# Kernel optimization log

Hardware: AMD Instinct MI355X
Metric: run time of the kernel (lower is better)

The kernel has to match this reference:

```python
import jax, jax.numpy as jnp
import numpy as np

B, C, L = 8, 128, 16384
K, STRIDE, PAD = 7, 3, 3
IC = 64  # intermediate_channels
CK = C * K  # 896 patch channels


def setup_inputs() -> dict:
    key = jax.random.key(0)
    ks = jax.random.split(key, 5)
    x = jax.random.normal(ks[0], (B, C, L), dtype=jnp.float32)
    W1 = jax.random.normal(ks[1], (IC, CK), dtype=jnp.float32) * (1.0 / np.sqrt(CK))
    b1 = jax.random.normal(ks[2], (IC,), dtype=jnp.float32) * 0.01
    W2 = jax.random.normal(ks[3], (CK, IC), dtype=jnp.float32) * (1.0 / np.sqrt(IC))
    b2 = jax.random.normal(ks[4], (CK,), dtype=jnp.float32) * 0.01
    return {"x": x, "W1": W1, "b1": b1, "W2": W2, "b2": b2}


def reference(x, W1, b1, W2, b2):
    b, c, l = x.shape
    lp = l + 2 * PAD
    # 1) circular pad along length
    xp = jnp.concatenate([x[..., -PAD:], x, x[..., :PAD]], axis=-1)  # (B,C,Lp)
    # 2) unfold: sliding windows of size K, stride STRIDE
    P = (lp - K) // STRIDE + 1
    idx = jnp.arange(P)[:, None] * STRIDE + jnp.arange(K)[None, :]  # (P,K)
    win = xp[:, :, idx]  # (B,C,P,K)
    # torch Unfold channel ordering: (B, C*K, P) with K fastest within channel
    patches = jnp.transpose(win, (0, 1, 3, 2)).reshape(b, c * K, P)
    # 3) 1x1-conv MLP on patch features
    h = jax.nn.relu(jnp.einsum('oc,bcp->bop', W1, patches) + b1[None, :, None])
    y = jnp.einsum('oc,bcp->bop', W2, h) + b2[None, :, None]  # (B, C*K, P)
    # 4) fold: overlap-add back to (B,C,Lp)
    vals = jnp.transpose(y.reshape(b, c, K, P), (0, 1, 3, 2))  # (B,C,P,K)
    folded = jnp.zeros((b, c, lp), dtype=x.dtype).at[:, :, idx].add(vals)
    # 5) ReplicationPad2d((0,0,1,1)) on height-1 tensor + mean over height=3:
    #    three identical rows averaged -> identity, preserved without materializing.
    # 6) crop back to original length
    return folded[:, :, PAD:PAD + l]
```

## Files before the change

### kernel.cpp

```cpp
#include <hip/hip_runtime.h>
#include <hip/hip_bf16.h>

#define B_    8
#define C_    128
#define L_    16384
#define K_    7
#define IC_   64
#define CK_   896
#define P_    5462
#define NP_   32
#define NT1_  171
#define NPOS_ 100
#define LDW_  136
#define HROWS 5480
#define HBSTR (HROWS * 64)

using bf16x8 = __attribute__((ext_vector_type(8))) __bf16;
using bf16x4 = __attribute__((ext_vector_type(4))) __bf16;
using f32x4  = __attribute__((ext_vector_type(4))) float;

#define W1KB_OFF  0
#define W2RB_OFF  114688
#define B2SUM_OFF 262144
#define B2TAB_OFF 263680
#define HTAB_OFF  270336

__global__ void prep_kernel(const float* __restrict__ W1, const float* __restrict__ W2,
                            const float* __restrict__ b2, __bf16* __restrict__ W1kb,
                            __bf16* __restrict__ W2rb, float* __restrict__ B2sum,
                            float* __restrict__ B2tab) {
    int idx = blockIdx.x * blockDim.x + threadIdx.x;
    int stride = gridDim.x * blockDim.x;
    for (int i = idx; i < 7 * 64 * 128; i += stride) {
        int k = i >> 13, o = (i >> 7) & 63, c = i & 127;
        W1kb[i] = (__bf16)W1[o * CK_ + c * 7 + k];
    }
    for (int i = idx; i < 3 * 128 * 3 * 64; i += stride) {
        int o = i & 63, t = (i >> 6) % 3, c = (i / 192) & 127, r = i / 24576;
        int kk = r + 3 * t;
        W2rb[i] = (kk <= 6) ? (__bf16)W2[(c * 7 + kk) * 64 + o] : (__bf16)0.0f;
    }
    for (int i = idx; i < 3 * 3 * 128; i += stride) {
        int c = i & 127, t = (i >> 7) % 3, r = i / 384;
        int kk = r + 3 * t;
        B2tab[i] = (kk <= 6) ? b2[c * 7 + kk] : 0.0f;
    }
    for (int i = idx; i < 3 * 128; i += stride) {
        int c = i & 127, r = i >> 7;
        float s = 0.0f;
        for (int t = 0; t < 3; ++t) { int kk = r + 3 * t; if (kk <= 6) s += b2[c * 7 + kk]; }
        B2sum[i] = s;
    }
}

__global__ __launch_bounds__(256, 4)
void conv1_kernel(const float* __restrict__ x, const float* __restrict__ b1,
                  const __bf16* __restrict__ W1kb, __bf16* __restrict__ hTab) {
    __shared__ __align__(16) __bf16 winT[NPOS_][LDW_];

    const int tid  = threadIdx.x;
    const int lane = tid & 63;
    const int w    = tid >> 6;
    const int row  = lane & 15;
    const int g    = lane >> 4;
    const int tile = blockIdx.x;
    const int b    = blockIdx.y;
    const int p0   = tile * NP_;
    const int gx0  = 3 * p0 - 3;

    __bf16* hb = hTab + (size_t)b * HBSTR;
    if (tile == 0 && tid < 64) reinterpret_cast<int*>(hb)[tid] = 0;

    const size_t xbase = ((size_t)b * C_) << 14;
    #pragma unroll
    for (int oc = 0; oc < 4; ++oc) {
        int c0 = (w * 4 + oc) * 8;
        const float* xr = x + xbase + ((size_t)c0 << 14);
        #pragma unroll
        for (int it = 0; it < 2; ++it) {
            int i = lane + (it << 6);
            if (i < NPOS_) {
                int xi = gx0 + i;
                xi += (xi < 0) ? L_ : 0;
                xi -= (xi >= L_) ? L_ : 0;
                bf16x8 pk;
                #pragma unroll
                for (int j = 0; j < 8; ++j)
                    pk[j] = (__bf16)xr[((size_t)j << 14) + xi];
                *reinterpret_cast<bf16x8*>(&winT[i][c0]) = pk;
            }
        }
    }

    __syncthreads();

    const bf16x8* W1v = reinterpret_cast<const bf16x8*>(W1kb);
    f32x4 acc1[2];
    #pragma unroll
    for (int pt = 0; pt < 2; ++pt) acc1[pt] = (f32x4){0.f, 0.f, 0.f, 0.f};
    #pragma unroll
    for (int k = 0; k < 7; ++k) {
        #pragma unroll
        for (int cs = 0; cs < 4; ++cs) {
            bf16x8 a = W1v[(k * 64 + w * 16 + row) * 16 + cs * 4 + g];
            #pragma unroll
            for (int pt = 0; pt < 2; ++pt) {
                const bf16x8 bfr = *reinterpret_cast<const bf16x8*>(
                    &winT[3 * (pt * 16 + row) + k][cs * 32 + g * 8]);
                acc1[pt] = __builtin_amdgcn_mfma_f32_16x16x32_bf16(a, bfr, acc1[pt], 0, 0, 0);
            }
        }
    }

    f32x4 b1v = *reinterpret_cast<const f32x4*>(b1 + w * 16 + g * 4);
    #pragma unroll
    for (int pt = 0; pt < 2; ++pt) {
        int pl = pt * 16 + row;
        int p  = p0 + pl;
        bool pvalid = (p < P_);
        bf16x4 hq;
        #pragma unroll
        for (int i = 0; i < 4; ++i) {
            float v = acc1[pt][i] + b1v[i];
            v = fmaxf(v, 0.0f);
            hq[i] = pvalid ? (__bf16)v : (__bf16)0.0f;
        }
        *reinterpret_cast<bf16x4*>(hb + (size_t)(p + 2) * 64 + w * 16 + g * 4) = hq;
    }
}

__global__ __launch_bounds__(256, 4)
void conv2_kernel(const __bf16* __restrict__ hTab, const __bf16* __restrict__ W2rb,
                  const float* __restrict__ B2sum, const float* __restrict__ B2tab,
                  float* __restrict__ out) {
    const int tid  = threadIdx.x;
    const int lane = tid & 63;
    const int w    = tid >> 6;
    const int row  = lane & 15;
    const int g    = lane >> 4;
    const int gx   = blockIdx.x;
    const int ch   = blockIdx.y;
    const int b    = blockIdx.z;

    const int ct = ch * 4 + w;
    const int c0 = ct * 16 + g * 4;

    const bf16x8* W2v = reinterpret_cast<const bf16x8*>(W2rb);
    bf16x8 af2[14];
    {
        int idx = 0;
        #pragma unroll
        for (int r = 0; r < 3; ++r) {
            const int ntt = (r == 0) ? 3 : 2;
            #pragma unroll
            for (int t = 0; t < 3; ++t) {
                if (t < ntt) {
                    #pragma unroll
                    for (int os = 0; os < 2; ++os) {
                        af2[idx] = W2v[((r * 128 + ct * 16 + row) * 3 + t) * 8 + os * 4 + g];
                        idx++;
                    }
                }
            }
        }
    }
    f32x4 bs[3];
    #pragma unroll
    for (int r = 0; r < 3; ++r)
        bs[r] = *reinterpret_cast<const f32x4*>(B2sum + r * 128 + c0);

    const __bf16* hb = hTab + (size_t)b * HBSTR;
    const size_t obase = ((size_t)b * C_) << 14;

    #pragma unroll
    for (int j = 0; j < 4; ++j) {
        const int qt = gx * 4 + j;
        const int q0 = qt * 16;
        if (q0 > P_) continue;

        bf16x8 bq[3][2];
        #pragma unroll
        for (int t = 0; t < 3; ++t)
            #pragma unroll
            for (int os = 0; os < 2; ++os)
                bq[t][os] = *reinterpret_cast<const bf16x8*>(
                    hb + (size_t)(q0 + row + 2 - t) * 64 + os * 32 + g * 8);

        const int q = q0 + row;
        f32x4 acc3[3];
        {
            int idx = 0;
            #pragma unroll
            for (int r = 0; r < 3; ++r) {
                acc3[r] = (f32x4){0.f, 0.f, 0.f, 0.f};
                const int ntt = (r == 0) ? 3 : 2;
                #pragma unroll
                for (int t = 0; t < 3; ++t) {
                    if (t < ntt) {
                        #pragma unroll
                        for (int os = 0; os < 2; ++os) {
                            acc3[r] = __builtin_amdgcn_mfma_f32_16x16x32_bf16(
                                af2[idx], bq[t][os], acc3[r], 0, 0, 0);
                            idx++;
                        }
                    }
                }
            }
        }

        const bool edge = (qt == 0) || (qt == 341);
        if (!edge) {
            #pragma unroll
            for (int i = 0; i < 4; ++i) {
                const int c = c0 + i;
                float* p = out + obase + (((size_t)c) << 14) + (3 * q - 3);
                p[0] = acc3[0][i] + bs[0][i];
                p[1] = acc3[1][i] + bs[1][i];
                p[2] = acc3[2][i] + bs[2][i];
            }
        } else {
            if (q >= 1 && q <= P_) {
                #pragma unroll
                for (int i = 0; i < 4; ++i) {
                    const int c = c0 + i;
                    float bv[3] = {0.f, 0.f, 0.f};
                    #pragma unroll
                    for (int r = 0; r < 3; ++r) {
                        const int ntt = (r == 0) ? 3 : 2;
                        #pragma unroll
                        for (int t = 0; t < 3; ++t) {
                            if (t < ntt && (unsigned)(q - t) < (unsigned)P_)
                                bv[r] += B2tab[(r * 3 + t) * 128 + c];
                        }
                    }
                    float* p = out + obase + (((size_t)c) << 14) + (3 * q - 3);
                    if (q <= P_ - 1) {
                        p[0] = acc3[0][i] + bv[0];
                        p[1] = acc3[1][i] + bv[1];
                        p[2] = acc3[2][i] + bv[2];
                    } else {
                        p[0] = acc3[0][i] + bv[0];
                    }
                }
            }
        }
    }
}

extern "C" void kernel_launch(void* const* d_in, const int* in_sizes, int n_in,
                              void* d_out, int out_size, void* d_ws, size_t ws_size,
                              hipStream_t stream) {
    const float* x  = (const float*)d_in[0];
    const float* W1 = (const float*)d_in[1];
    const float* b1 = (const float*)d_in[2];
    const float* W2 = (const float*)d_in[3];
    const float* b2 = (const float*)d_in[4];
    float* out = (float*)d_out;
    char* ws = (char*)d_ws;
    __bf16* W1kb = (__bf16*)(ws + W1KB_OFF);
    __bf16* W2rb = (__bf16*)(ws + W2RB_OFF);
    float* B2sum = (float*)(ws + B2SUM_OFF);
    float* B2tab = (float*)(ws + B2TAB_OFF);
    __bf16* hTab = (__bf16*)(ws + HTAB_OFF);

    prep_kernel<<<64, 256, 0, stream>>>(W1, W2, b2, W1kb, W2rb, B2sum, B2tab);
    conv1_kernel<<<dim3(NT1_, B_), 256, 0, stream>>>(x, b1, W1kb, hTab);
    conv2_kernel<<<dim3(86, 2, B_), 256, 0, stream>>>(hTab, W2rb, B2sum, B2tab, out);
}
```

Measured before the change: 82.42 us.

## Halve conv1 tile size and load x with vectorized float4 channel-pair reads

Conv1 now covers 16 patches per block instead of 32, doubling the grid and raising the occupancy hint to 8 blocks per SM. The x staging loop changes from scalar per-position strided loads to float4 loads along length for pairs of channels, writing bf16 pairs into the transposed shared window. The goal is better global load coalescing and more parallelism. The cost is more halo overlap between tiles and fewer MFMAs per block to amortise the W1 fragment loads.

```diff
diff --git a/kernel.cpp b/kernel.cpp
--- a/kernel.cpp
+++ b/kernel.cpp
@@ -8,15 +8,16 @@
 #define IC_   64
 #define CK_   896
 #define P_    5462
-#define NP_   32
-#define NT1_  171
-#define NPOS_ 100
+#define NP_   16
+#define NT1_  342
+#define NPOS_ 52
 #define LDW_  136
 #define HROWS 5480
 #define HBSTR (HROWS * 64)
 
 using bf16x8 = __attribute__((ext_vector_type(8))) __bf16;
 using bf16x4 = __attribute__((ext_vector_type(4))) __bf16;
+using bf16x2 = __attribute__((ext_vector_type(2))) __bf16;
 using f32x4  = __attribute__((ext_vector_type(4))) float;
 
 #define W1KB_OFF  0
@@ -53,7 +54,7 @@
     }
 }
 
-__global__ __launch_bounds__(256, 4)
+__global__ __launch_bounds__(256, 8)
 void conv1_kernel(const float* __restrict__ x, const float* __restrict__ b1,
                   const __bf16* __restrict__ W1kb, __bf16* __restrict__ hTab) {
     __shared__ __align__(16) __bf16 winT[NPOS_][LDW_];
@@ -67,27 +68,32 @@
     const int b    = blockIdx.y;
     const int p0   = tile * NP_;
     const int gx0  = 3 * p0 - 3;
+    const int ax0  = gx0 - 1;
 
     __bf16* hb = hTab + (size_t)b * HBSTR;
     if (tile == 0 && tid < 64) reinterpret_cast<int*>(hb)[tid] = 0;
 
     const size_t xbase = ((size_t)b * C_) << 14;
-    #pragma unroll
-    for (int oc = 0; oc < 4; ++oc) {
-        int c0 = (w * 4 + oc) * 8;
-        const float* xr = x + xbase + ((size_t)c0 << 14);
-        #pragma unroll
-        for (int it = 0; it < 2; ++it) {
-            int i = lane + (it << 6);
-            if (i < NPOS_) {
-                int xi = gx0 + i;
+    {
+        const int c2 = lane * 2;
+        const float* xr0 = x + xbase + ((size_t)c2 << 14);
+        #pragma unroll
+        for (int jq = 0; jq < 4; ++jq) {
+            int q = w * 4 + jq;
+            if (q < 14) {
+                int xi = ax0 + q * 4;
                 xi += (xi < 0) ? L_ : 0;
                 xi -= (xi >= L_) ? L_ : 0;
-                bf16x8 pk;
+                f32x4 va = *reinterpret_cast<const f32x4*>(xr0 + xi);
+                f32x4 vb = *reinterpret_cast<const f32x4*>(xr0 + L_ + xi);
                 #pragma unroll
-                for (int j = 0; j < 8; ++j)
-                    pk[j] = (__bf16)xr[((size_t)j << 14) + xi];
-                *reinterpret_cast<bf16x8*>(&winT[i][c0]) = pk;
+                for (int j = 0; j < 4; ++j) {
+                    int pos = q * 4 + j - 1;
+                    if ((unsigned)pos < (unsigned)NPOS_) {
+                        bf16x2 pk; pk[0] = (__bf16)va[j]; pk[1] = (__bf16)vb[j];
+                        *reinterpret_cast<bf16x2*>(&winT[pos][c2]) = pk;
+                    }
+                }
             }
         }
     }
@@ -95,33 +101,26 @@
     __syncthreads();
 
     const bf16x8* W1v = reinterpret_cast<const bf16x8*>(W1kb);
-    f32x4 acc1[2];
-    #pragma unroll
-    for (int pt = 0; pt < 2; ++pt) acc1[pt] = (f32x4){0.f, 0.f, 0.f, 0.f};
+    f32x4 acc1 = (f32x4){0.f, 0.f, 0.f, 0.f};
     #pragma unroll
     for (int k = 0; k < 7; ++k) {
         #pragma unroll
         for (int cs = 0; cs < 4; ++cs) {
             bf16x8 a = W1v[(k * 64 + w * 16 + row) * 16 + cs * 4 + g];
-            #pragma unroll
-            for (int pt = 0; pt < 2; ++pt) {
-                const bf16x8 bfr = *reinterpret_cast<const bf16x8*>(
-                    &winT[3 * (pt * 16 + row) + k][cs * 32 + g * 8]);
-                acc1[pt] = __builtin_amdgcn_mfma_f32_16x16x32_bf16(a, bfr, acc1[pt], 0, 0, 0);
-            }
+            const bf16x8 bfr = *reinterpret_cast<const bf16x8*>(
+                &winT[3 * row + k][cs * 32 + g * 8]);
+            acc1 = __builtin_amdgcn_mfma_f32_16x16x32_bf16(a, bfr, acc1, 0, 0, 0);
         }
     }
 
     f32x4 b1v = *reinterpret_cast<const f32x4*>(b1 + w * 16 + g * 4);
-    #pragma unroll
-    for (int pt = 0; pt < 2; ++pt) {
-        int pl = pt * 16 + row;
-        int p  = p0 + pl;
+    {
+        int p = p0 + row;
         bool pvalid = (p < P_);
         bf16x4 hq;
         #pragma unroll
         for (int i = 0; i < 4; ++i) {
-            float v = acc1[pt][i] + b1v[i];
+            float v = acc1[i] + b1v[i];
             v = fmaxf(v, 0.0f);
             hq[i] = pvalid ? (__bf16)v : (__bf16)0.0f;
         }
```

New measurement: 102.5 us. 24.4% more time.

## Coalesce conv1 window loads with float2 per-channel rows and XOR-swizzled LDS

Applied to the files above, without the earlier changes.

The conv1 staging loop now has each lane load a float2 of two adjacent positions along one channel row, instead of gathering 8 channels per position with strided scalar loads. Writes into the LDS window use an XOR swizzle on the channel index, and the MFMA B-fragment reads apply the same swizzle to limit bank conflicts. Occupancy hint is raised to 5 blocks per CU. conv2 q-tiling is shifted by one, and the tail hTab rows are zeroed to cover the shifted edge. This risks edge-case correctness and extra register pressure in exchange for better global coalescing.

```diff
diff --git a/kernel.cpp b/kernel.cpp
--- a/kernel.cpp
+++ b/kernel.cpp
@@ -53,10 +53,10 @@
     }
 }
 
-__global__ __launch_bounds__(256, 4)
+__global__ __launch_bounds__(256, 5)
 void conv1_kernel(const float* __restrict__ x, const float* __restrict__ b1,
                   const __bf16* __restrict__ W1kb, __bf16* __restrict__ hTab) {
-    __shared__ __align__(16) __bf16 winT[NPOS_][LDW_];
+    __shared__ __align__(16) __bf16 winT[NPOS_ * LDW_];
 
     const int tid  = threadIdx.x;
     const int lane = tid & 63;
@@ -67,27 +67,33 @@
     const int b    = blockIdx.y;
     const int p0   = tile * NP_;
     const int gx0  = 3 * p0 - 3;
+    const int ax2  = gx0 - 1;
 
     __bf16* hb = hTab + (size_t)b * HBSTR;
     if (tile == 0 && tid < 64) reinterpret_cast<int*>(hb)[tid] = 0;
+    if (tile == NT1_ - 1 && tid < 192) reinterpret_cast<int*>(hb + 5474 * 64)[tid] = 0;
 
     const size_t xbase = ((size_t)b * C_) << 14;
-    #pragma unroll
-    for (int oc = 0; oc < 4; ++oc) {
-        int c0 = (w * 4 + oc) * 8;
-        const float* xr = x + xbase + ((size_t)c0 << 14);
-        #pragma unroll
-        for (int it = 0; it < 2; ++it) {
-            int i = lane + (it << 6);
-            if (i < NPOS_) {
-                int xi = gx0 + i;
-                xi += (xi < 0) ? L_ : 0;
-                xi -= (xi >= L_) ? L_ : 0;
-                bf16x8 pk;
-                #pragma unroll
-                for (int j = 0; j < 8; ++j)
-                    pk[j] = (__bf16)xr[((size_t)j << 14) + xi];
-                *reinterpret_cast<bf16x8*>(&winT[i][c0]) = pk;
+    {
+        int xi = ax2 + 2 * lane;
+        xi += (xi < 0) ? L_ : 0;
+        xi -= (xi >= L_) ? L_ : 0;
+        const bool ld = (lane <= 50);
+        const bool wA = (lane >= 1);
+        const bool wB = (lane <= 49);
+        const int posA = 2 * lane - 1, posB = 2 * lane;
+        const int kA8 = ((posA >> 3) & 7) << 3;
+        const int kB8 = ((posB >> 3) & 7) << 3;
+        const int baseA = posA * LDW_;
+        const int baseB = posB * LDW_;
+        const float* xr = x + xbase + xi;
+        #pragma unroll 8
+        for (int rr = 0; rr < 32; ++rr) {
+            const int c = w * 32 + rr;
+            if (ld) {
+                float2 v = *reinterpret_cast<const float2*>(xr + ((size_t)c << 14));
+                if (wA) winT[baseA + (c ^ kA8)] = (__bf16)v.x;
+                if (wB) winT[baseB + (c ^ kB8)] = (__bf16)v.y;
             }
         }
     }
@@ -105,8 +111,9 @@
             bf16x8 a = W1v[(k * 64 + w * 16 + row) * 16 + cs * 4 + g];
             #pragma unroll
             for (int pt = 0; pt < 2; ++pt) {
-                const bf16x8 bfr = *reinterpret_cast<const bf16x8*>(
-                    &winT[3 * (pt * 16 + row) + k][cs * 32 + g * 8]);
+                const int pos = 3 * (pt * 16 + row) + k;
+                const int el  = (cs * 32 + g * 8) ^ (((pos >> 3) & 7) << 3);
+                const bf16x8 bfr = *reinterpret_cast<const bf16x8*>(&winT[pos * LDW_ + el]);
                 acc1[pt] = __builtin_amdgcn_mfma_f32_16x16x32_bf16(a, bfr, acc1[pt], 0, 0, 0);
             }
         }
@@ -115,8 +122,7 @@
     f32x4 b1v = *reinterpret_cast<const f32x4*>(b1 + w * 16 + g * 4);
     #pragma unroll
     for (int pt = 0; pt < 2; ++pt) {
-        int pl = pt * 16 + row;
-        int p  = p0 + pl;
+        int p = p0 + pt * 16 + row;
         bool pvalid = (p < P_);
         bf16x4 hq;
         #pragma unroll
@@ -175,7 +181,7 @@
     #pragma unroll
     for (int j = 0; j < 4; ++j) {
         const int qt = gx * 4 + j;
-        const int q0 = qt * 16;
+        const int q0 = qt * 16 + 1;
         if (q0 > P_) continue;
 
         bf16x8 bq[3][2];
@@ -219,7 +225,7 @@
                 p[2] = acc3[2][i] + bs[2][i];
             }
         } else {
-            if (q >= 1 && q <= P_) {
+            if (q <= P_) {
                 #pragma unroll
                 for (int i = 0; i < 4; ++i) {
                     const int c = c0 + i;
```

New measurement: 89.32 us. +8.4%, slower.
